# Kernel tuning notes

Hardware: AMD Instinct MI355X
Metric: run time of the kernel (lower is better)

The kernel has to match this reference:

```python
import jax, jax.numpy as jnp
import numpy as np

B, E, S, DIM, HID, H = 8, 512, 1024, 1024, 1024, 8  # S == DIM == HID by construction


def setup_inputs() -> dict:
    key = jax.random.key(0)
    ks = jax.random.split(key, 7)
    x = jax.random.normal(ks[0], (B, E, S), dtype=jnp.float32)
    # per-head projection Linear(dim, hidden_dim): weight [H, hidden, dim], bias [H, hidden]
    proj_w = jax.random.normal(ks[1], (H, HID, DIM), dtype=jnp.float32) / np.sqrt(DIM)
    proj_b = jax.random.normal(ks[2], (H, HID), dtype=jnp.float32) * 0.02
    # per-head ColRepeatCausalLinear: weight [H, S] (torch.randn(1, dim)), bias [H, S] (zeros init)
    mix_w = jax.random.normal(ks[3], (H, S), dtype=jnp.float32)
    mix_b = jnp.zeros((H, S), dtype=jnp.float32)
    # out_proj Linear(dim, dim)
    out_w = jax.random.normal(ks[4], (DIM, DIM), dtype=jnp.float32) / np.sqrt(DIM)
    out_b = jax.random.normal(ks[5], (DIM,), dtype=jnp.float32) * 0.02
    return {"x": x, "proj_w": proj_w, "proj_b": proj_b, "mix_w": mix_w,
            "mix_b": mix_b, "out_w": out_w, "out_b": out_b, "index": 0}


def reference(x, proj_w, proj_b, mix_w, mix_b, out_w, out_b, index):
    # Per-head linear projection on the last axis (grouped GEMM across heads).
    # proj: [B, H, E, HID]
    proj = jnp.einsum('bes,hds->bhed', x, proj_w) + proj_b[None, :, None, :]
    # ColRepeatCausalLinear parallel path with decay_value == 1:
    # W[i, j] = v[j] for j >= i  =>  (x @ W)[..., j] = v[j] * cumsum(x, -1)[..., j]
    mixed = mix_w[None, :, None, :] * jnp.cumsum(proj, axis=-1) + mix_b[None, :, None, :]
    # torch.cat(activations, dim=1): [B, H*E, S]
    hidden = mixed.reshape(B, H * E, S)
    # out_proj Linear(dim, dim) on last axis
    out = hidden @ out_w.T + out_b
    return out
```

## Files before the change

### kernel.cpp

```cpp
#include <hip/hip_runtime.h>

#define NH    8
#define NE    512
#define NB    8
#define ND    1024
#define NROW  4096

typedef unsigned short u16;
typedef __attribute__((ext_vector_type(8))) short short8;
typedef __attribute__((ext_vector_type(4))) float f32x4;

__device__ __forceinline__ u16 f2bf(float f) {
  unsigned int u = __float_as_uint(f);
  u += 0x7fffu + ((u >> 16) & 1u);
  return (u16)(u >> 16);
}

__device__ __forceinline__ void gload16(const u16* g, u16* l) {
  __builtin_amdgcn_global_load_lds(
      (const __attribute__((address_space(1))) unsigned int*)(const void*)g,
      (__attribute__((address_space(3))) unsigned int*)(void*)l, 16, 0, 0);
}

__global__ __launch_bounds__(256) void convert_x_kernel(const float* __restrict__ X,
                                                        u16* __restrict__ Xb) {
  int i = blockIdx.x * 256 + threadIdx.x;
  float4 v = ((const float4*)X)[i];
  ushort4 o;
  o.x = f2bf(v.x); o.y = f2bf(v.y); o.z = f2bf(v.z); o.w = f2bf(v.w);
  ((ushort4*)Xb)[i] = o;
}

__global__ __launch_bounds__(256) void transpose_w_kernel(const float* __restrict__ W,
                                                          u16* __restrict__ Wt) {
  __shared__ float tile[64][65];
  int h  = blockIdx.z;
  int s0 = blockIdx.x * 64;
  int d0 = blockIdx.y * 64;
  int t  = threadIdx.x;
  int tr = t >> 4;
  int tc = t & 15;
#pragma unroll
  for (int i = 0; i < 4; ++i) {
    int d = tr + i * 16;
    float4 v = *(const float4*)(W + ((size_t)h * ND + d0 + d) * ND + s0 + tc * 4);
    tile[d][tc * 4 + 0] = v.x;
    tile[d][tc * 4 + 1] = v.y;
    tile[d][tc * 4 + 2] = v.z;
    tile[d][tc * 4 + 3] = v.w;
  }
  __syncthreads();
#pragma unroll
  for (int i = 0; i < 4; ++i) {
    int s  = tr + i * 16;
    int dd = tc * 4;
    ushort4 o;
    o.x = f2bf(tile[dd + 0][s]);
    o.y = f2bf(tile[dd + 1][s]);
    o.z = f2bf(tile[dd + 2][s]);
    o.w = f2bf(tile[dd + 3][s]);
    *(ushort4*)(Wt + ((size_t)h * ND + s0 + s) * ND + d0 + dd) = o;
  }
}

__global__ __launch_bounds__(256) void scan_kernel(const float* __restrict__ out_w,
                                                   const float* __restrict__ mix_w,
                                                   const float* __restrict__ mix_b,
                                                   const float* __restrict__ proj_b,
                                                   const float* __restrict__ out_b,
                                                   u16* __restrict__ Afac,
                                                   float* __restrict__ Kc) {
  int h = blockIdx.x >> 10;
  int o = blockIdx.x & 1023;
  int t = threadIdx.x;
  int lane = t & 63, wave = t >> 6;
  const float* owr = out_w + (size_t)o * ND;
  const float* mwr = mix_w + (size_t)h * ND;
  const float* mbr = mix_b + (size_t)h * ND;
  const float* pbr = proj_b + (size_t)h * ND;

  float l[4];
  float run = 0.f, mbdot = 0.f;
#pragma unroll
  for (int k = 0; k < 4; ++k) {
    int j = 1023 - (4 * t + k);
    float ow = owr[j];
    mbdot += ow * mbr[j];
    run += ow * mwr[j];
    l[k] = run;
  }
  float tsum = run;
  float sc = tsum;
#pragma unroll
  for (int d = 1; d < 64; d <<= 1) {
    float other = __shfl_up(sc, d);
    if (lane >= d) sc += other;
  }
  __shared__ float wsum[4];
  __shared__ float red[4];
  if (lane == 63) wsum[wave] = sc;
  __syncthreads();
  float wprefix = 0.f;
  for (int w = 0; w < wave; ++w) wprefix += wsum[w];
  float excl = wprefix + sc - tsum;

  float cdot = 0.f;
  ushort4 pack;
  u16* pk = (u16*)&pack;
#pragma unroll
  for (int k = 0; k < 4; ++k) {
    int d = 1023 - (4 * t + k);
    float a = excl + l[k];
    cdot += a * pbr[d];
    pk[3 - k] = f2bf(a);
  }
  *(ushort4*)(Afac + ((size_t)(h * ND + o)) * ND + (1020 - 4 * t)) = pack;

  float tot = cdot + mbdot;
#pragma unroll
  for (int m = 32; m >= 1; m >>= 1) tot += __shfl_xor(tot, m);
  if (lane == 0) red[wave] = tot;
  __syncthreads();
  if (t == 0) {
    Kc[h * ND + o] = red[0] + red[1] + red[2] + red[3] + out_b[o];
  }
}

__device__ __forceinline__ void gemm_core(const u16* __restrict__ Ag,
                                          const u16* __restrict__ Bg,
                                          u16* As, u16* Bs,
                                          f32x4 acc[4][4]) {
  const int t    = threadIdx.x;
  const int lane = t & 63;
  const int wave = t >> 6;
  const int wm   = (wave >> 1) * 64;
  const int wn   = (wave & 1) * 64;
  const int row0 = t >> 2;
  const int kc0  = (t & 3) * 8;
  u16* dA0 = As + t * 8;
  u16* dA1 = As + 2048 + t * 8;
  u16* dB0 = Bs + t * 8;
  u16* dB1 = Bs + 2048 + t * 8;
  const int arow  = wm + (lane & 15);
  const int brow  = wn + (lane & 15);
  const int kfrag = (lane >> 4) * 8;

  for (int kk = 0; kk < 1024; kk += 32) {
    __syncthreads();
    gload16(Ag + (size_t)row0 * 1024 + kk + kc0, dA0);
    gload16(Ag + (size_t)(row0 + 64) * 1024 + kk + kc0, dA1);
    gload16(Bg + (size_t)row0 * 1024 + kk + kc0, dB0);
    gload16(Bg + (size_t)(row0 + 64) * 1024 + kk + kc0, dB1);
    __syncthreads();
    short8 af[4], bf[4];
#pragma unroll
    for (int mi = 0; mi < 4; ++mi)
      af[mi] = *(const short8*)(As + (arow + mi * 16) * 32 + kfrag);
#pragma unroll
    for (int ni = 0; ni < 4; ++ni)
      bf[ni] = *(const short8*)(Bs + (brow + ni * 16) * 32 + kfrag);
#pragma unroll
    for (int mi = 0; mi < 4; ++mi)
#pragma unroll
      for (int ni = 0; ni < 4; ++ni)
        acc[mi][ni] = __builtin_amdgcn_mfma_f32_16x16x32_bf16(af[mi], bf[ni], acc[mi][ni], 0, 0, 0);
  }
}

__global__ __launch_bounds__(256) void gemm1_kernel(const u16* __restrict__ Afac,
                                                    const u16* __restrict__ Wt,
                                                    u16* __restrict__ Mmat) {
  __shared__ __align__(16) u16 As[128 * 32];
  __shared__ __align__(16) u16 Bs[128 * 32];
  int h  = blockIdx.z;
  int m0 = blockIdx.y * 128;
  int n0 = blockIdx.x * 128;
  const u16* Ag = Afac + ((size_t)h * ND + m0) * ND;
  const u16* Bg = Wt + ((size_t)h * ND + n0) * ND;
  f32x4 acc[4][4];
  f32x4 z = {0.f, 0.f, 0.f, 0.f};
#pragma unroll
  for (int i = 0; i < 4; ++i)
#pragma unroll
    for (int j = 0; j < 4; ++j) acc[i][j] = z;
  gemm_core(Ag, Bg, As, Bs, acc);

  const int lane = threadIdx.x & 63;
  const int wave = threadIdx.x >> 6;
  const int wm = (wave >> 1) * 64, wn = (wave & 1) * 64;
  int r0 = m0 + wm + ((lane >> 4) << 2);
  int c0 = n0 + wn + (lane & 15);
  u16* Mh = Mmat + (size_t)h * ND * ND;
#pragma unroll
  for (int mi = 0; mi < 4; ++mi)
#pragma unroll
    for (int ni = 0; ni < 4; ++ni)
#pragma unroll
      for (int r = 0; r < 4; ++r)
        Mh[(size_t)(r0 + mi * 16 + r) * ND + c0 + ni * 16] = f2bf(acc[mi][ni][r]);
}

#define MFMA_(d, a, b) d = __builtin_amdgcn_mfma_f32_16x16x32_bf16(a, b, d, 0, 0, 0)
#define NOVM ((void)0)
#define VM6 asm volatile("s_waitcnt vmcnt(6)" ::: "memory")
#define VM0 asm volatile("s_waitcnt vmcnt(0)" ::: "memory")

#define PHASE(q, b, STAGE_STMT, VMSTMT) do {                                   \
    short8 a00 = ldA(b, 2*(q),     0);                                         \
    short8 a01 = ldA(b, 2*(q),     1);                                         \
    short8 a10 = ldA(b, 2*(q) + 1, 0);                                         \
    short8 a11 = ldA(b, 2*(q) + 1, 1);                                         \
    if ((q) == 0) {                                                            \
      bf00 = ldB(b, 0, 0); bf01 = ldB(b, 0, 1);                                \
      bf10 = ldB(b, 1, 0); bf11 = ldB(b, 1, 1);                                \
      bf20 = ldB(b, 2, 0); bf21 = ldB(b, 2, 1);                                \
      bf30 = ldB(b, 3, 0); bf31 = ldB(b, 3, 1);                                \
    }                                                                          \
    STAGE_STMT;                                                                \
    __builtin_amdgcn_sched_barrier(0);                                         \
    VMSTMT;                                                                    \
    __builtin_amdgcn_s_barrier();                                              \
    asm volatile("s_waitcnt lgkmcnt(0)" ::: "memory");                         \
    __builtin_amdgcn_sched_barrier(0);                                         \
    __builtin_amdgcn_s_setprio(1);                                             \
    MFMA_(acc[2*(q)  ][0], a00, bf00);                                         \
    MFMA_(acc[2*(q)  ][1], a00, bf10);                                         \
    MFMA_(acc[2*(q)  ][2], a00, bf20);                                         \
    MFMA_(acc[2*(q)  ][3], a00, bf30);                                         \
    MFMA_(acc[2*(q)+1][0], a10, bf00);                                         \
    MFMA_(acc[2*(q)+1][1], a10, bf10);                                         \
    MFMA_(acc[2*(q)+1][2], a10, bf20);                                         \
    MFMA_(acc[2*(q)+1][3], a10, bf30);                                         \
    MFMA_(acc[2*(q)  ][0], a01, bf01);                                         \
    MFMA_(acc[2*(q)  ][1], a01, bf11);                                         \
    MFMA_(acc[2*(q)  ][2], a01, bf21);                                         \
    MFMA_(acc[2*(q)  ][3], a01, bf31);                                         \
    MFMA_(acc[2*(q)+1][0], a11, bf01);                                         \
    MFMA_(acc[2*(q)+1][1], a11, bf11);                                         \
    MFMA_(acc[2*(q)+1][2], a11, bf21);                                         \
    MFMA_(acc[2*(q)+1][3], a11, bf31);                                         \
    __builtin_amdgcn_s_setprio(0);                                             \
    __builtin_amdgcn_s_barrier();                                              \
  } while (0)

__global__ __launch_bounds__(512, 2) void gemm2_8ph(const u16* __restrict__ Xb,
                                                    const u16* __restrict__ Bm,
                                                    const float* __restrict__ Kc,
                                                    float* __restrict__ Out) {
  __shared__ __align__(16) u16 lds[65536];
  const int tid  = threadIdx.x;
  const int lane = tid & 63;
  const int wave = tid >> 6;
  const int wm   = wave >> 2;
  const int wn   = wave & 3;

  int bid = blockIdx.x;
  int swz = (bid & 7) * 64 + (bid >> 3);
  int m0  = (swz >> 5) * 256;
  int n0  = (swz & 31) * 256;

  const int li8 = lane >> 3;
  const int lc  = (lane & 7) ^ li8;
  const size_t stSrc = (size_t)li8 * ND + lc * 8;
  const int stDst = lane * 8;

  const u16* aSrc = Xb + (size_t)m0 * ND + stSrc;
  const u16* bSrc = Bm + (size_t)n0 * ND + stSrc;

  const int fr  = lane & 15;
  const int ca0 = (((lane >> 4)    ) ^ (lane & 7)) * 8;
  const int ca1 = (((lane >> 4) + 4) ^ (lane & 7)) * 8;
  const int aOff = (wm * 128 + fr) * 64;
  const int bOff = 16384 + (wn * 64 + fr) * 64;

  auto stageA = [&](int h, int t, int b) {
#pragma unroll
    for (int jj = 0; jj < 2; ++jj) {
      int j = 2 * wave + jj;
      int R = ((j >> 3) << 7) + h * 64 + ((j & 7) << 3);
      gload16(aSrc + (size_t)R * ND + t * 64, lds + b * 32768 + R * 64 + stDst);
    }
  };
  auto stageB = [&](int h, int t, int b) {
#pragma unroll
    for (int jj = 0; jj < 2; ++jj) {
      int j = 2 * wave + jj;
      int R = h * 128 + j * 8;
      gload16(bSrc + (size_t)R * ND + t * 64, lds + b * 32768 + 16384 + R * 64 + stDst);
    }
  };
  auto ldA = [&](int b, int mi, int kk) -> short8 {
    return *(const short8*)(lds + b * 32768 + aOff + mi * 1024 + (kk ? ca1 : ca0));
  };
  auto ldB = [&](int b, int ni, int kk) -> short8 {
    return *(const short8*)(lds + b * 32768 + bOff + ni * 1024 + (kk ? ca1 : ca0));
  };

  f32x4 acc[8][4];
  f32x4 z = {0.f, 0.f, 0.f, 0.f};
#pragma unroll
  for (int i = 0; i < 8; ++i)
#pragma unroll
    for (int j = 0; j < 4; ++j) acc[i][j] = z;

  short8 bf00, bf01, bf10, bf11, bf20, bf21, bf30, bf31;

  stageA(0, 0, 0); stageA(1, 0, 0);
  stageB(0, 0, 0); stageB(1, 0, 0);
  stageB(0, 1, 1); stageB(1, 1, 1);
  stageA(0, 1, 1);
  asm volatile("s_waitcnt vmcnt(6)" ::: "memory");
  __builtin_amdgcn_s_barrier();

#pragma unroll 1
  for (int it = 0; it < 7; ++it) {
    const int T = 2 * it;
    PHASE(0, 0, stageA(1, T + 1, 1), NOVM);
    PHASE(1, 0, stageB(0, T + 2, 0), NOVM);
    PHASE(2, 0, stageB(1, T + 2, 0), NOVM);
    PHASE(3, 0, stageA(0, T + 2, 0), VM6);
    PHASE(0, 1, stageA(1, T + 2, 0), NOVM);
    PHASE(1, 1, stageB(0, T + 3, 1), NOVM);
    PHASE(2, 1, stageB(1, T + 3, 1), NOVM);
    PHASE(3, 1, stageA(0, T + 3, 1), VM6);
  }
  PHASE(0, 0, stageA(1, 15, 1), NOVM);
  PHASE(1, 0, NOVM, NOVM);
  PHASE(2, 0, NOVM, NOVM);
  PHASE(3, 0, NOVM, VM0);
  PHASE(0, 1, NOVM, NOVM);
  PHASE(1, 1, NOVM, NOVM);
  PHASE(2, 1, NOVM, NOVM);
  PHASE(3, 1, NOVM, NOVM);

  const int hH = n0 >> 10;
  const int r0 = m0 + wm * 128 + ((lane >> 4) << 2);
  const int c0 = n0 + wn * 64 + fr;
  const int o0 = c0 & 1023;
  float bias[4];
#pragma unroll
  for (int ni = 0; ni < 4; ++ni) bias[ni] = Kc[c0 + ni * 16];
#pragma unroll
  for (int mi = 0; mi < 8; ++mi) {
#pragma unroll
    for (int r = 0; r < 4; ++r) {
      int rb = r0 + mi * 16 + r;
      float* orow = Out + ((size_t)(rb >> 9) * 4096 + hH * 512 + (rb & 511)) * 1024 + o0;
#pragma unroll
      for (int ni = 0; ni < 4; ++ni)
        orow[ni * 16] = acc[mi][ni][r] + bias[ni];
    }
  }
}

extern "C" void kernel_launch(void* const* d_in, const int* in_sizes, int n_in,
                              void* d_out, int out_size, void* d_ws, size_t ws_size,
                              hipStream_t stream) {
  (void)in_sizes; (void)n_in; (void)out_size; (void)ws_size;
  const float* x      = (const float*)d_in[0];
  const float* proj_w = (const float*)d_in[1];
  const float* proj_b = (const float*)d_in[2];
  const float* mix_w  = (const float*)d_in[3];
  const float* mix_b  = (const float*)d_in[4];
  const float* out_w  = (const float*)d_in[5];
  const float* out_b  = (const float*)d_in[6];
  float* Out = (float*)d_out;

  u16* Wt   = (u16*)d_out;
  u16* Afac = (u16*)d_out + (size_t)8 * 1024 * 1024;
  u16*   Xb   = (u16*)d_ws;
  u16*   Mmat = (u16*)((char*)d_ws + ((size_t)8 << 20));
  float* Kc   = (float*)((char*)d_ws + ((size_t)24 << 20));

  convert_x_kernel<<<4096, 256, 0, stream>>>(x, Xb);
  transpose_w_kernel<<<dim3(16, 16, NH), 256, 0, stream>>>(proj_w, Wt);
  scan_kernel<<<NH * ND, 256, 0, stream>>>(out_w, mix_w, mix_b, proj_b, out_b, Afac, Kc);
  gemm1_kernel<<<dim3(8, 8, NH), 256, 0, stream>>>(Afac, Wt, Mmat);
  gemm2_8ph<<<512, 512, 0, stream>>>(Xb, Mmat, Kc, Out);
}
```

Before: 133.8 us.

## Stage gemm1 epilogue through LDS and make gemm2 blocks compute two N tiles

The gemm1 epilogue now writes its bf16 results into a swizzled shared-memory tile, then stores them to global memory as coalesced 16-byte vectors instead of scattered 2-byte stores. gemm2 now launches 256 blocks, and each block loops over two adjacent 256-column tiles with a new XCD-aware mapping. This keeps the same A rows hot in cache and cuts the block count to about one wave at 2 blocks per CU. The risks are an extra 32KB of LDS in gemm1, which can lower its occupancy, and serialised work per block in gemm2 with no overlap between the two halves.

```diff
diff --git a/kernel.cpp b/kernel.cpp
--- a/kernel.cpp
+++ b/kernel.cpp
@@ -172,6 +172,7 @@
                                                     u16* __restrict__ Mmat) {
   __shared__ __align__(16) u16 As[128 * 32];
   __shared__ __align__(16) u16 Bs[128 * 32];
+  __shared__ __align__(16) u16 Cs[128 * 128];
   int h  = blockIdx.z;
   int m0 = blockIdx.y * 128;
   int n0 = blockIdx.x * 128;
@@ -185,19 +186,34 @@
     for (int j = 0; j < 4; ++j) acc[i][j] = z;
   gemm_core(Ag, Bg, As, Bs, acc);
 
-  const int lane = threadIdx.x & 63;
-  const int wave = threadIdx.x >> 6;
+  const int t    = threadIdx.x;
+  const int lane = t & 63;
+  const int wave = t >> 6;
   const int wm = (wave >> 1) * 64, wn = (wave & 1) * 64;
-  int r0 = m0 + wm + ((lane >> 4) << 2);
-  int c0 = n0 + wn + (lane & 15);
+  const int rg = lane >> 4;
+  const int fr = lane & 15;
+#pragma unroll
+  for (int mi = 0; mi < 4; ++mi)
+#pragma unroll
+    for (int ni = 0; ni < 4; ++ni)
+#pragma unroll
+      for (int r = 0; r < 4; ++r) {
+        int rl = wm + mi * 16 + rg * 4 + r;
+        int c  = wn + ni * 16 + fr;
+        Cs[rl * 128 + 8 * ((c >> 3) ^ (rl & 7)) + (c & 7)] = f2bf(acc[mi][ni][r]);
+      }
+  __syncthreads();
   u16* Mh = Mmat + (size_t)h * ND * ND;
 #pragma unroll
-  for (int mi = 0; mi < 4; ++mi)
-#pragma unroll
-    for (int ni = 0; ni < 4; ++ni)
-#pragma unroll
-      for (int r = 0; r < 4; ++r)
-        Mh[(size_t)(r0 + mi * 16 + r) * ND + c0 + ni * 16] = f2bf(acc[mi][ni][r]);
+  for (int rr = 0; rr < 4; ++rr) {
+    int rl = rr * 32 + (t >> 3);
+#pragma unroll
+    for (int j = 0; j < 2; ++j) {
+      int c8 = (t & 7) + 8 * j;
+      short8 v = *(const short8*)(Cs + rl * 128 + 8 * (c8 ^ (rl & 7)));
+      *(short8*)(Mh + (size_t)(m0 + rl) * ND + n0 + c8 * 8) = v;
+    }
+  }
 }
 
 #define MFMA_(d, a, b) d = __builtin_amdgcn_mfma_f32_16x16x32_bf16(a, b, d, 0, 0, 0)
@@ -254,10 +270,12 @@
   const int wm   = wave >> 2;
   const int wn   = wave & 3;
 
-  int bid = blockIdx.x;
-  int swz = (bid & 7) * 64 + (bid >> 3);
-  int m0  = (swz >> 5) * 256;
-  int n0  = (swz & 31) * 256;
+  const int bid   = blockIdx.x;
+  const int xcd   = bid & 7;
+  const int loc   = bid >> 3;
+  const int mb    = (xcd >> 2) * 8 + (loc >> 2);
+  const int npair = (xcd & 3) * 4 + (loc & 3);
+  const int m0    = mb * 256;
 
   const int li8 = lane >> 3;
   const int lc  = (lane & 7) ^ li8;
@@ -265,30 +283,18 @@
   const int stDst = lane * 8;
 
   const u16* aSrc = Xb + (size_t)m0 * ND + stSrc;
-  const u16* bSrc = Bm + (size_t)n0 * ND + stSrc;
 
   const int fr  = lane & 15;
+  const int rg  = lane >> 4;
   const int ca0 = (((lane >> 4)    ) ^ (lane & 7)) * 8;
   const int ca1 = (((lane >> 4) + 4) ^ (lane & 7)) * 8;
   const int aOff = (wm * 128 + fr) * 64;
   const int bOff = 16384 + (wn * 64 + fr) * 64;
 
-  auto stageA = [&](int h, int t, int b) {
-#pragma unroll
-    for (int jj = 0; jj < 2; ++jj) {
-      int j = 2 * wave + jj;
-      int R = ((j >> 3) << 7) + h * 64 + ((j & 7) << 3);
-      gload16(aSrc + (size_t)R * ND + t * 64, lds + b * 32768 + R * 64 + stDst);
-    }
-  };
-  auto stageB = [&](int h, int t, int b) {
-#pragma unroll
-    for (int jj = 0; jj < 2; ++jj) {
-      int j = 2 * wave + jj;
-      int R = h * 128 + j * 8;
-      gload16(bSrc + (size_t)R * ND + t * 64, lds + b * 32768 + 16384 + R * 64 + stDst);
-    }
-  };
+  f32x4 acc[8][4];
+  const f32x4 z = {0.f, 0.f, 0.f, 0.f};
+  short8 bf00, bf01, bf10, bf11, bf20, bf21, bf30, bf31;
+
   auto ldA = [&](int b, int mi, int kk) -> short8 {
     return *(const short8*)(lds + b * 32768 + aOff + mi * 1024 + (kk ? ca1 : ca0));
   };
@@ -296,59 +302,77 @@
     return *(const short8*)(lds + b * 32768 + bOff + ni * 1024 + (kk ? ca1 : ca0));
   };
 
-  f32x4 acc[8][4];
-  f32x4 z = {0.f, 0.f, 0.f, 0.f};
-#pragma unroll
-  for (int i = 0; i < 8; ++i)
-#pragma unroll
-    for (int j = 0; j < 4; ++j) acc[i][j] = z;
-
-  short8 bf00, bf01, bf10, bf11, bf20, bf21, bf30, bf31;
-
-  stageA(0, 0, 0); stageA(1, 0, 0);
-  stageB(0, 0, 0); stageB(1, 0, 0);
-  stageB(0, 1, 1); stageB(1, 1, 1);
-  stageA(0, 1, 1);
-  asm volatile("s_waitcnt vmcnt(6)" ::: "memory");
-  __builtin_amdgcn_s_barrier();
-
 #pragma unroll 1
-  for (int it = 0; it < 7; ++it) {
-    const int T = 2 * it;
-    PHASE(0, 0, stageA(1, T + 1, 1), NOVM);
-    PHASE(1, 0, stageB(0, T + 2, 0), NOVM);
-    PHASE(2, 0, stageB(1, T + 2, 0), NOVM);
-    PHASE(3, 0, stageA(0, T + 2, 0), VM6);
-    PHASE(0, 1, stageA(1, T + 2, 0), NOVM);
-    PHASE(1, 1, stageB(0, T + 3, 1), NOVM);
-    PHASE(2, 1, stageB(1, T + 3, 1), NOVM);
-    PHASE(3, 1, stageA(0, T + 3, 1), VM6);
-  }
-  PHASE(0, 0, stageA(1, 15, 1), NOVM);
-  PHASE(1, 0, NOVM, NOVM);
-  PHASE(2, 0, NOVM, NOVM);
-  PHASE(3, 0, NOVM, VM0);
-  PHASE(0, 1, NOVM, NOVM);
-  PHASE(1, 1, NOVM, NOVM);
-  PHASE(2, 1, NOVM, NOVM);
-  PHASE(3, 1, NOVM, NOVM);
-
-  const int hH = n0 >> 10;
-  const int r0 = m0 + wm * 128 + ((lane >> 4) << 2);
-  const int c0 = n0 + wn * 64 + fr;
-  const int o0 = c0 & 1023;
-  float bias[4];
-#pragma unroll
-  for (int ni = 0; ni < 4; ++ni) bias[ni] = Kc[c0 + ni * 16];
-#pragma unroll
-  for (int mi = 0; mi < 8; ++mi) {
-#pragma unroll
-    for (int r = 0; r < 4; ++r) {
-      int rb = r0 + mi * 16 + r;
-      float* orow = Out + ((size_t)(rb >> 9) * 4096 + hH * 512 + (rb & 511)) * 1024 + o0;
-#pragma unroll
-      for (int ni = 0; ni < 4; ++ni)
-        orow[ni * 16] = acc[mi][ni][r] + bias[ni];
+  for (int hf = 0; hf < 2; ++hf) {
+    const int n0 = npair * 512 + hf * 256;
+    const u16* bSrc = Bm + (size_t)n0 * ND + stSrc;
+
+    auto stageA = [&](int h, int t, int b) {
+#pragma unroll
+      for (int jj = 0; jj < 2; ++jj) {
+        int j = 2 * wave + jj;
+        int R = ((j >> 3) << 7) + h * 64 + ((j & 7) << 3);
+        gload16(aSrc + (size_t)R * ND + t * 64, lds + b * 32768 + R * 64 + stDst);
+      }
+    };
+    auto stageB = [&](int h, int t, int b) {
+#pragma unroll
+      for (int jj = 0; jj < 2; ++jj) {
+        int j = 2 * wave + jj;
+        int R = h * 128 + j * 8;
+        gload16(bSrc + (size_t)R * ND + t * 64, lds + b * 32768 + 16384 + R * 64 + stDst);
+      }
+    };
+
+#pragma unroll
+    for (int i = 0; i < 8; ++i)
+#pragma unroll
+      for (int j = 0; j < 4; ++j) acc[i][j] = z;
+
+    stageA(0, 0, 0); stageA(1, 0, 0);
+    stageB(0, 0, 0); stageB(1, 0, 0);
+    stageB(0, 1, 1); stageB(1, 1, 1);
+    stageA(0, 1, 1);
+    VM6;
+    __builtin_amdgcn_s_barrier();
+
+#pragma unroll 1
+    for (int it = 0; it < 7; ++it) {
+      const int T = 2 * it;
+      PHASE(0, 0, stageA(1, T + 1, 1), NOVM);
+      PHASE(1, 0, stageB(0, T + 2, 0), NOVM);
+      PHASE(2, 0, stageB(1, T + 2, 0), NOVM);
+      PHASE(3, 0, stageA(0, T + 2, 0), VM6);
+      PHASE(0, 1, stageA(1, T + 2, 0), NOVM);
+      PHASE(1, 1, stageB(0, T + 3, 1), NOVM);
+      PHASE(2, 1, stageB(1, T + 3, 1), NOVM);
+      PHASE(3, 1, stageA(0, T + 3, 1), VM6);
+    }
+    PHASE(0, 0, stageA(1, 15, 1), NOVM);
+    PHASE(1, 0, NOVM, NOVM);
+    PHASE(2, 0, NOVM, NOVM);
+    PHASE(3, 0, NOVM, VM0);
+    PHASE(0, 1, NOVM, NOVM);
+    PHASE(1, 1, NOVM, NOVM);
+    PHASE(2, 1, NOVM, NOVM);
+    PHASE(3, 1, NOVM, NOVM);
+
+    const int hH = n0 >> 10;
+    const int o0 = (n0 & 1023) + wn * 64 + fr;
+    const int r0 = m0 + wm * 128 + rg * 4;
+    float bias[4];
+#pragma unroll
+    for (int ni = 0; ni < 4; ++ni) bias[ni] = Kc[hH * 1024 + o0 + ni * 16];
+#pragma unroll
+    for (int mi = 0; mi < 8; ++mi) {
+#pragma unroll
+      for (int r = 0; r < 4; ++r) {
+        int rb = r0 + mi * 16 + r;
+        float* orow = Out + ((size_t)(rb >> 9) * 4096 + hH * 512 + (rb & 511)) * 1024 + o0;
+#pragma unroll
+        for (int ni = 0; ni < 4; ++ni)
+          orow[ni * 16] = acc[mi][ni][r] + bias[ni];
+      }
     }
   }
 }
@@ -376,5 +400,5 @@
   transpose_w_kernel<<<dim3(16, 16, NH), 256, 0, stream>>>(proj_w, Wt);
   scan_kernel<<<NH * ND, 256, 0, stream>>>(out_w, mix_w, mix_b, proj_b, out_b, Afac, Kc);
   gemm1_kernel<<<dim3(8, 8, NH), 256, 0, stream>>>(Afac, Wt, Mmat);
-  gemm2_8ph<<<512, 512, 0, stream>>>(Xb, Mmat, Kc, Out);
-}
+  gemm2_8ph<<<256, 512, 0, stream>>>(Xb, Mmat, Kc, Out);
+}
```

New measurement: 150.0 us. 1.12x slower.

## Reuse pipelined 8-phase 256x256 GEMM core for the weight-folding GEMM

Applied to the files above, without the earlier changes.

Replaces the simple 128x128 single-buffered gemm1 kernel, which syncs twice per 32-wide K step, with the same double-buffered, swizzled-LDS, 8-phase MFMA pipeline already used by gemm2. The shared body moves into a macro used by both kernels. This cuts barrier stalls and raises data reuse per tile for the 8 per-head 1024^3 GEMMs. In exchange, the grid shrinks to 128 blocks of 512 threads, which may underfill the CUs.

```diff
diff --git a/kernel.cpp b/kernel.cpp
--- a/kernel.cpp
+++ b/kernel.cpp
@@ -124,80 +124,6 @@
   if (t == 0) {
     Kc[h * ND + o] = red[0] + red[1] + red[2] + red[3] + out_b[o];
   }
-}
-
-__device__ __forceinline__ void gemm_core(const u16* __restrict__ Ag,
-                                          const u16* __restrict__ Bg,
-                                          u16* As, u16* Bs,
-                                          f32x4 acc[4][4]) {
-  const int t    = threadIdx.x;
-  const int lane = t & 63;
-  const int wave = t >> 6;
-  const int wm   = (wave >> 1) * 64;
-  const int wn   = (wave & 1) * 64;
-  const int row0 = t >> 2;
-  const int kc0  = (t & 3) * 8;
-  u16* dA0 = As + t * 8;
-  u16* dA1 = As + 2048 + t * 8;
-  u16* dB0 = Bs + t * 8;
-  u16* dB1 = Bs + 2048 + t * 8;
-  const int arow  = wm + (lane & 15);
-  const int brow  = wn + (lane & 15);
-  const int kfrag = (lane >> 4) * 8;
-
-  for (int kk = 0; kk < 1024; kk += 32) {
-    __syncthreads();
-    gload16(Ag + (size_t)row0 * 1024 + kk + kc0, dA0);
-    gload16(Ag + (size_t)(row0 + 64) * 1024 + kk + kc0, dA1);
-    gload16(Bg + (size_t)row0 * 1024 + kk + kc0, dB0);
-    gload16(Bg + (size_t)(row0 + 64) * 1024 + kk + kc0, dB1);
-    __syncthreads();
-    short8 af[4], bf[4];
-#pragma unroll
-    for (int mi = 0; mi < 4; ++mi)
-      af[mi] = *(const short8*)(As + (arow + mi * 16) * 32 + kfrag);
-#pragma unroll
-    for (int ni = 0; ni < 4; ++ni)
-      bf[ni] = *(const short8*)(Bs + (brow + ni * 16) * 32 + kfrag);
-#pragma unroll
-    for (int mi = 0; mi < 4; ++mi)
-#pragma unroll
-      for (int ni = 0; ni < 4; ++ni)
-        acc[mi][ni] = __builtin_amdgcn_mfma_f32_16x16x32_bf16(af[mi], bf[ni], acc[mi][ni], 0, 0, 0);
-  }
-}
-
-__global__ __launch_bounds__(256) void gemm1_kernel(const u16* __restrict__ Afac,
-                                                    const u16* __restrict__ Wt,
-                                                    u16* __restrict__ Mmat) {
-  __shared__ __align__(16) u16 As[128 * 32];
-  __shared__ __align__(16) u16 Bs[128 * 32];
-  int h  = blockIdx.z;
-  int m0 = blockIdx.y * 128;
-  int n0 = blockIdx.x * 128;
-  const u16* Ag = Afac + ((size_t)h * ND + m0) * ND;
-  const u16* Bg = Wt + ((size_t)h * ND + n0) * ND;
-  f32x4 acc[4][4];
-  f32x4 z = {0.f, 0.f, 0.f, 0.f};
-#pragma unroll
-  for (int i = 0; i < 4; ++i)
-#pragma unroll
-    for (int j = 0; j < 4; ++j) acc[i][j] = z;
-  gemm_core(Ag, Bg, As, Bs, acc);
-
-  const int lane = threadIdx.x & 63;
-  const int wave = threadIdx.x >> 6;
-  const int wm = (wave >> 1) * 64, wn = (wave & 1) * 64;
-  int r0 = m0 + wm + ((lane >> 4) << 2);
-  int c0 = n0 + wn + (lane & 15);
-  u16* Mh = Mmat + (size_t)h * ND * ND;
-#pragma unroll
-  for (int mi = 0; mi < 4; ++mi)
-#pragma unroll
-    for (int ni = 0; ni < 4; ++ni)
-#pragma unroll
-      for (int r = 0; r < 4; ++r)
-        Mh[(size_t)(r0 + mi * 16 + r) * ND + c0 + ni * 16] = f2bf(acc[mi][ni][r]);
 }
 
 #define MFMA_(d, a, b) d = __builtin_amdgcn_mfma_f32_16x16x32_bf16(a, b, d, 0, 0, 0)
@@ -243,98 +169,117 @@
     __builtin_amdgcn_s_barrier();                                              \
   } while (0)
 
+#define GEMM_8PH_BODY(ASRC, BSRC)                                              \
+  const int tid  = threadIdx.x;                                                \
+  const int lane = tid & 63;                                                   \
+  const int wave = tid >> 6;                                                   \
+  const int wm   = wave >> 2;                                                  \
+  const int wn   = wave & 3;                                                   \
+  const int li8 = lane >> 3;                                                   \
+  const int lc  = (lane & 7) ^ li8;                                            \
+  const size_t stSrc = (size_t)li8 * ND + lc * 8;                              \
+  const int stDst = lane * 8;                                                  \
+  const u16* aSrc = (ASRC) + stSrc;                                            \
+  const u16* bSrc = (BSRC) + stSrc;                                            \
+  const int fr  = lane & 15;                                                   \
+  const int rg  = lane >> 4;                                                   \
+  const int ca0 = (((lane >> 4)    ) ^ (lane & 7)) * 8;                        \
+  const int ca1 = (((lane >> 4) + 4) ^ (lane & 7)) * 8;                        \
+  const int aOff = (wm * 128 + fr) * 64;                                       \
+  const int bOff = 16384 + (wn * 64 + fr) * 64;                                \
+  auto stageA = [&](int h, int t, int b) {                                     \
+    _Pragma("unroll")                                                          \
+    for (int jj = 0; jj < 2; ++jj) {                                           \
+      int j = 2 * wave + jj;                                                   \
+      int R = ((j >> 3) << 7) + h * 64 + ((j & 7) << 3);                       \
+      gload16(aSrc + (size_t)R * ND + t * 64, lds + b * 32768 + R * 64 + stDst); \
+    }                                                                          \
+  };                                                                           \
+  auto stageB = [&](int h, int t, int b) {                                     \
+    _Pragma("unroll")                                                          \
+    for (int jj = 0; jj < 2; ++jj) {                                           \
+      int j = 2 * wave + jj;                                                   \
+      int R = h * 128 + j * 8;                                                 \
+      gload16(bSrc + (size_t)R * ND + t * 64, lds + b * 32768 + 16384 + R * 64 + stDst); \
+    }                                                                          \
+  };                                                                           \
+  auto ldA = [&](int b, int mi, int kk) -> short8 {                            \
+    return *(const short8*)(lds + b * 32768 + aOff + mi * 1024 + (kk ? ca1 : ca0)); \
+  };                                                                           \
+  auto ldB = [&](int b, int ni, int kk) -> short8 {                            \
+    return *(const short8*)(lds + b * 32768 + bOff + ni * 1024 + (kk ? ca1 : ca0)); \
+  };                                                                           \
+  f32x4 acc[8][4];                                                             \
+  f32x4 z = {0.f, 0.f, 0.f, 0.f};                                              \
+  _Pragma("unroll")                                                            \
+  for (int i = 0; i < 8; ++i)                                                  \
+    _Pragma("unroll")                                                          \
+    for (int j = 0; j < 4; ++j) acc[i][j] = z;                                 \
+  short8 bf00, bf01, bf10, bf11, bf20, bf21, bf30, bf31;                       \
+  stageA(0, 0, 0); stageA(1, 0, 0);                                            \
+  stageB(0, 0, 0); stageB(1, 0, 0);                                            \
+  stageB(0, 1, 1); stageB(1, 1, 1);                                            \
+  stageA(0, 1, 1);                                                             \
+  asm volatile("s_waitcnt vmcnt(6)" ::: "memory");                             \
+  __builtin_amdgcn_s_barrier();                                                \
+  _Pragma("unroll 1")                                                          \
+  for (int it = 0; it < 7; ++it) {                                             \
+    const int T = 2 * it;                                                      \
+    PHASE(0, 0, stageA(1, T + 1, 1), NOVM);                                    \
+    PHASE(1, 0, stageB(0, T + 2, 0), NOVM);                                    \
+    PHASE(2, 0, stageB(1, T + 2, 0), NOVM);                                    \
+    PHASE(3, 0, stageA(0, T + 2, 0), VM6);                                     \
+    PHASE(0, 1, stageA(1, T + 2, 0), NOVM);                                    \
+    PHASE(1, 1, stageB(0, T + 3, 1), NOVM);                                    \
+    PHASE(2, 1, stageB(1, T + 3, 1), NOVM);                                    \
+    PHASE(3, 1, stageA(0, T + 3, 1), VM6);                                     \
+  }                                                                            \
+  PHASE(0, 0, stageA(1, 15, 1), NOVM);                                         \
+  PHASE(1, 0, NOVM, NOVM);                                                     \
+  PHASE(2, 0, NOVM, NOVM);                                                     \
+  PHASE(3, 0, NOVM, VM0);                                                      \
+  PHASE(0, 1, NOVM, NOVM);                                                     \
+  PHASE(1, 1, NOVM, NOVM);                                                     \
+  PHASE(2, 1, NOVM, NOVM);                                                     \
+  PHASE(3, 1, NOVM, NOVM);
+
+__global__ __launch_bounds__(512, 2) void gemm1_8ph(const u16* __restrict__ Afac,
+                                                    const u16* __restrict__ Wt,
+                                                    u16* __restrict__ Mmat) {
+  __shared__ __align__(16) u16 lds[65536];
+  const int h  = blockIdx.z;
+  const int m0 = blockIdx.y * 256;
+  const int n0 = blockIdx.x * 256;
+  GEMM_8PH_BODY(Afac + ((size_t)h * ND + m0) * ND, Wt + ((size_t)h * ND + n0) * ND)
+
+  u16* Mh = Mmat + (size_t)h * ND * ND;
+  const int r0 = m0 + wm * 128 + rg * 4;
+  const int c0 = n0 + wn * 64 + fr;
+#pragma unroll
+  for (int mi = 0; mi < 8; ++mi) {
+#pragma unroll
+    for (int r = 0; r < 4; ++r) {
+      u16* orow = Mh + (size_t)(r0 + mi * 16 + r) * ND + c0;
+#pragma unroll
+      for (int ni = 0; ni < 4; ++ni)
+        orow[ni * 16] = f2bf(acc[mi][ni][r]);
+    }
+  }
+}
+
 __global__ __launch_bounds__(512, 2) void gemm2_8ph(const u16* __restrict__ Xb,
                                                     const u16* __restrict__ Bm,
                                                     const float* __restrict__ Kc,
                                                     float* __restrict__ Out) {
   __shared__ __align__(16) u16 lds[65536];
-  const int tid  = threadIdx.x;
-  const int lane = tid & 63;
-  const int wave = tid >> 6;
-  const int wm   = wave >> 2;
-  const int wn   = wave & 3;
-
-  int bid = blockIdx.x;
-  int swz = (bid & 7) * 64 + (bid >> 3);
-  int m0  = (swz >> 5) * 256;
-  int n0  = (swz & 31) * 256;
-
-  const int li8 = lane >> 3;
-  const int lc  = (lane & 7) ^ li8;
-  const size_t stSrc = (size_t)li8 * ND + lc * 8;
-  const int stDst = lane * 8;
-
-  const u16* aSrc = Xb + (size_t)m0 * ND + stSrc;
-  const u16* bSrc = Bm + (size_t)n0 * ND + stSrc;
-
-  const int fr  = lane & 15;
-  const int ca0 = (((lane >> 4)    ) ^ (lane & 7)) * 8;
-  const int ca1 = (((lane >> 4) + 4) ^ (lane & 7)) * 8;
-  const int aOff = (wm * 128 + fr) * 64;
-  const int bOff = 16384 + (wn * 64 + fr) * 64;
-
-  auto stageA = [&](int h, int t, int b) {
-#pragma unroll
-    for (int jj = 0; jj < 2; ++jj) {
-      int j = 2 * wave + jj;
-      int R = ((j >> 3) << 7) + h * 64 + ((j & 7) << 3);
-      gload16(aSrc + (size_t)R * ND + t * 64, lds + b * 32768 + R * 64 + stDst);
-    }
-  };
-  auto stageB = [&](int h, int t, int b) {
-#pragma unroll
-    for (int jj = 0; jj < 2; ++jj) {
-      int j = 2 * wave + jj;
-      int R = h * 128 + j * 8;
-      gload16(bSrc + (size_t)R * ND + t * 64, lds + b * 32768 + 16384 + R * 64 + stDst);
-    }
-  };
-  auto ldA = [&](int b, int mi, int kk) -> short8 {
-    return *(const short8*)(lds + b * 32768 + aOff + mi * 1024 + (kk ? ca1 : ca0));
-  };
-  auto ldB = [&](int b, int ni, int kk) -> short8 {
-    return *(const short8*)(lds + b * 32768 + bOff + ni * 1024 + (kk ? ca1 : ca0));
-  };
-
-  f32x4 acc[8][4];
-  f32x4 z = {0.f, 0.f, 0.f, 0.f};
-#pragma unroll
-  for (int i = 0; i < 8; ++i)
-#pragma unroll
-    for (int j = 0; j < 4; ++j) acc[i][j] = z;
-
-  short8 bf00, bf01, bf10, bf11, bf20, bf21, bf30, bf31;
-
-  stageA(0, 0, 0); stageA(1, 0, 0);
-  stageB(0, 0, 0); stageB(1, 0, 0);
-  stageB(0, 1, 1); stageB(1, 1, 1);
-  stageA(0, 1, 1);
-  asm volatile("s_waitcnt vmcnt(6)" ::: "memory");
-  __builtin_amdgcn_s_barrier();
-
-#pragma unroll 1
-  for (int it = 0; it < 7; ++it) {
-    const int T = 2 * it;
-    PHASE(0, 0, stageA(1, T + 1, 1), NOVM);
-    PHASE(1, 0, stageB(0, T + 2, 0), NOVM);
-    PHASE(2, 0, stageB(1, T + 2, 0), NOVM);
-    PHASE(3, 0, stageA(0, T + 2, 0), VM6);
-    PHASE(0, 1, stageA(1, T + 2, 0), NOVM);
-    PHASE(1, 1, stageB(0, T + 3, 1), NOVM);
-    PHASE(2, 1, stageB(1, T + 3, 1), NOVM);
-    PHASE(3, 1, stageA(0, T + 3, 1), VM6);
-  }
-  PHASE(0, 0, stageA(1, 15, 1), NOVM);
-  PHASE(1, 0, NOVM, NOVM);
-  PHASE(2, 0, NOVM, NOVM);
-  PHASE(3, 0, NOVM, VM0);
-  PHASE(0, 1, NOVM, NOVM);
-  PHASE(1, 1, NOVM, NOVM);
-  PHASE(2, 1, NOVM, NOVM);
-  PHASE(3, 1, NOVM, NOVM);
+  const int bid = blockIdx.x;
+  const int swz = (bid & 7) * 64 + (bid >> 3);
+  const int m0  = (swz >> 5) * 256;
+  const int n0  = (swz & 31) * 256;
+  GEMM_8PH_BODY(Xb + (size_t)m0 * ND, Bm + (size_t)n0 * ND)
 
   const int hH = n0 >> 10;
-  const int r0 = m0 + wm * 128 + ((lane >> 4) << 2);
+  const int r0 = m0 + wm * 128 + rg * 4;
   const int c0 = n0 + wn * 64 + fr;
   const int o0 = c0 & 1023;
   float bias[4];
@@ -375,6 +320,6 @@
   convert_x_kernel<<<4096, 256, 0, stream>>>(x, Xb);
   transpose_w_kernel<<<dim3(16, 16, NH), 256, 0, stream>>>(proj_w, Wt);
   scan_kernel<<<NH * ND, 256, 0, stream>>>(out_w, mix_w, mix_b, proj_b, out_b, Afac, Kc);
-  gemm1_kernel<<<dim3(8, 8, NH), 256, 0, stream>>>(Afac, Wt, Mmat);
+  gemm1_8ph<<<dim3(4, 4, NH), 512, 0, stream>>>(Afac, Wt, Mmat);
   gemm2_8ph<<<512, 512, 0, stream>>>(Xb, Mmat, Kc, Out);
 }
```

New measurement: 131.8 us. No clear change (-1.5%).
